# Performance work log

Hardware: AMD Instinct MI355X
Metric: run time of the kernel (lower is better)

## Reference

```python
import jax, jax.numpy as jnp
import numpy as np

N_EMBED = 192
N_HEAD = 6
HEAD_DIM = N_EMBED // N_HEAD  # 32


def setup_inputs() -> dict:
    key = jax.random.key(0)
    k1, k2, k3, k4, k5 = jax.random.split(key, 5)
    B, T = 2048, 128
    scale_qkv = 1.0 / np.sqrt(N_EMBED)
    return {
        "x": jax.random.normal(k1, (B, T, N_EMBED), dtype=jnp.float32),
        "w_qkv": jax.random.normal(k2, (N_EMBED, 3 * N_EMBED), dtype=jnp.float32) * scale_qkv,
        "b_qkv": jax.random.normal(k3, (3 * N_EMBED,), dtype=jnp.float32) * 0.01,
        "w_proj": jax.random.normal(k4, (N_EMBED, N_EMBED), dtype=jnp.float32) * scale_qkv,
        "b_proj": jax.random.normal(k5, (N_EMBED,), dtype=jnp.float32) * 0.01,
    }


def reference(x, w_qkv, b_qkv, w_proj, b_proj):
    B, T, C = x.shape
    qkv = x @ w_qkv + b_qkv                       # [B, T, 3C]
    q, k, v = jnp.split(qkv, 3, axis=-1)
    # [B, H, T, D]
    def heads(t):
        return t.reshape(B, T, N_HEAD, HEAD_DIM).transpose(0, 2, 1, 3)
    q, k, v = heads(q), heads(k), heads(v)
    att = jnp.einsum("bhtd,bhsd->bhts", q, k) / np.sqrt(HEAD_DIM).astype(x.dtype)
    causal = jnp.tril(jnp.ones((T, T), dtype=bool))
    att = jnp.where(causal, att, jnp.finfo(att.dtype).min)
    att = jax.nn.softmax(att, axis=-1)
    # dropout is identity in eval mode
    y = jnp.einsum("bhts,bhsd->bhtd", att, v)      # [B, H, T, D]
    y = y.transpose(0, 2, 1, 3).reshape(B, T, C)
    return y @ w_proj + b_proj
```

## Files before the change

kernel.cpp:

```cpp
#include <hip/hip_runtime.h>
#include <hip/hip_bf16.h>

#define T_  128
#define C_  192
#define H_  6
#define C3_ 576
#define SLAB_ELEMS (96 * 192)
#define SLAB_BYTES (SLAB_ELEMS * 2)

typedef __bf16 bf16x8 __attribute__((ext_vector_type(8)));
typedef __bf16 bf16x4 __attribute__((ext_vector_type(4)));
typedef float  f32x4  __attribute__((ext_vector_type(4)));
typedef unsigned short u16;

__global__ void prep_weights(const float* __restrict__ w_qkv,
                             const float* __restrict__ w_proj,
                             u16* __restrict__ wt)
{
    int idx = blockIdx.x * 256 + threadIdx.x;
    if (idx >= 8 * SLAB_ELEMS) return;
    int slab = idx / SLAB_ELEMS;
    int rem  = idx % SLAB_ELEMS;
    int nl   = rem / 192;
    int kkp  = rem % 192;
    int d    = kkp ^ ((nl & 7) << 3);
    int kt   = d >> 5;
    int e    = d & 31;
    int g    = e >> 3;
    int r    = e & 7;
    int hi   = r >> 2;
    int i    = r & 3;
    int k    = kt * 32 + hi * 16 + g * 4 + i;
    float v;
    if (slab < 6) {
        int sec = nl >> 5;
        int col = sec * C_ + slab * 32 + (nl & 31);
        v = w_qkv[(size_t)k * C3_ + col];
    } else {
        int col = (slab - 6) * 96 + nl;
        v = w_proj[(size_t)k * C_ + col];
    }
    __bf16 bv = (__bf16)v;
    wt[idx] = *reinterpret_cast<u16*>(&bv);
}

__device__ __forceinline__ bf16x8 ld_frag(const __bf16* p) {
    union { bf16x8 v; struct { bf16x4 lo, hi; } s; } u;
    u.s.lo = *reinterpret_cast<const bf16x4*>(p);
    u.s.hi = *reinterpret_cast<const bf16x4*>(p + 16);
    return u.v;
}

__device__ __forceinline__ bf16x8 ld_w(const __bf16* wl, int nl, int kt, int g) {
    return *reinterpret_cast<const bf16x8*>(
        &wl[nl * 192 + (((kt << 5) + (g << 3)) ^ ((nl & 7) << 3))]);
}

__device__ __forceinline__ void stage_slab(const u16* __restrict__ src, u16* dst,
                                           int wid, int lane) {
    #pragma unroll
    for (int p = 0; p < 4; ++p) {
        int off = p * 4096 + wid * 512;
        __builtin_amdgcn_global_load_lds(
            (const __attribute__((address_space(1))) void*)(src + off + lane * 8),
            (__attribute__((address_space(3))) void*)(dst + off), 16, 0, 0);
    }
    if (wid < 4) {
        int off = 16384 + wid * 512;
        __builtin_amdgcn_global_load_lds(
            (const __attribute__((address_space(1))) void*)(src + off + lane * 8),
            (__attribute__((address_space(3))) void*)(dst + off), 16, 0, 0);
    }
}

__global__ __launch_bounds__(512, 4) void attn_fused(
    const float* __restrict__ x,
    const u16*   __restrict__ wt,
    const float* __restrict__ b_qkv,
    const float* __restrict__ b_proj,
    float* __restrict__ y)
{
    __shared__ __align__(16) u16   w_lds[SLAB_ELEMS];
    __shared__ __align__(16) __bf16 k_s[128][40];
    __shared__ __align__(16) __bf16 vt_s[32][136];

    const __bf16* wl = reinterpret_cast<const __bf16*>(w_lds);

    const int b    = blockIdx.x;
    const int tid  = threadIdx.x;
    const int wid  = tid >> 6;
    const int lane = tid & 63;
    const int li   = lane & 15;
    const int g    = lane >> 4;
    const int trow = 16 * wid;
    const int tq   = trow + li;

    const float scale = 0.17677669529663687f;

    stage_slab(wt, w_lds, wid, lane);

    bf16x8 xf[6];
    {
        const float* xr = x + ((size_t)b * T_ + tq) * C_;
        #pragma unroll
        for (int kt = 0; kt < 6; ++kt) {
            f32x4 a0 = *reinterpret_cast<const f32x4*>(xr + kt*32 + 4*g);
            f32x4 a1 = *reinterpret_cast<const f32x4*>(xr + kt*32 + 16 + 4*g);
            bf16x8 f;
            f[0] = (__bf16)a0[0]; f[1] = (__bf16)a0[1]; f[2] = (__bf16)a0[2]; f[3] = (__bf16)a0[3];
            f[4] = (__bf16)a1[0]; f[5] = (__bf16)a1[1]; f[6] = (__bf16)a1[2]; f[7] = (__bf16)a1[3];
            xf[kt] = f;
        }
    }

    bf16x8 of[6];

    #pragma unroll
    for (int h = 0; h < H_; ++h) {
        __syncthreads();

        f32x4 qacc0, qacc1;
        #pragma unroll
        for (int nt = 0; nt < 6; ++nt) {
            const int sec = nt >> 1;
            const int nl  = nt * 16 + li;
            f32x4 acc = *reinterpret_cast<const f32x4*>(
                &b_qkv[sec * C_ + h * 32 + (nt & 1) * 16 + 4 * g]);
            #pragma unroll
            for (int kt = 0; kt < 6; ++kt)
                acc = __builtin_amdgcn_mfma_f32_16x16x32_bf16(ld_w(wl, nl, kt, g),
                                                              xf[kt], acc, 0, 0, 0);
            if (nt == 0)      qacc0 = acc;
            else if (nt == 1) qacc1 = acc;
            else if (nt < 4) {
                bf16x4 pk;
                pk[0]=(__bf16)acc[0]; pk[1]=(__bf16)acc[1]; pk[2]=(__bf16)acc[2]; pk[3]=(__bf16)acc[3];
                *reinterpret_cast<bf16x4*>(&k_s[tq][(nt & 1)*16 + 4*g]) = pk;
            } else {
                #pragma unroll
                for (int r = 0; r < 4; ++r)
                    vt_s[(nt & 1)*16 + 4*g + r][tq] = (__bf16)acc[r];
            }
        }
        bf16x8 qf;
        #pragma unroll
        for (int j = 0; j < 4; ++j) {
            qf[j]     = (__bf16)qacc0[j];
            qf[4 + j] = (__bf16)qacc1[j];
        }
        __syncthreads();

        stage_slab(wt + (h + 1) * SLAB_ELEMS, w_lds, wid, lane);

        float l = 0.f;
        f32x4 o0 = {0.f,0.f,0.f,0.f}, o1 = {0.f,0.f,0.f,0.f};
        #pragma unroll
        for (int hh = 0; hh < 2; ++hh) {
            if (hh == 1 && wid < 4) break;
            f32x4 sacc[4];
            #pragma unroll
            for (int j = 0; j < 4; ++j) {
                bf16x8 kf = ld_frag(&k_s[(hh*4 + j)*16 + li][4*g]);
                f32x4 z = {0.f, 0.f, 0.f, 0.f};
                sacc[j] = __builtin_amdgcn_mfma_f32_16x16x32_bf16(kf, qf, z, 0, 0, 0);
            }
            #pragma unroll
            for (int j = 0; j < 4; ++j) {
                #pragma unroll
                for (int r = 0; r < 4; ++r) {
                    const int key = (hh*4 + j)*16 + 4*g + r;
                    float p = (key <= tq) ? __expf(sacc[j][r] * scale) : 0.f;
                    sacc[j][r] = p;
                    l += p;
                }
            }
            #pragma unroll
            for (int kp = 0; kp < 2; ++kp) {
                bf16x8 pf;
                #pragma unroll
                for (int j2 = 0; j2 < 4; ++j2) {
                    pf[j2]     = (__bf16)sacc[2*kp][j2];
                    pf[4 + j2] = (__bf16)sacc[2*kp + 1][j2];
                }
                bf16x8 vf0 = ld_frag(&vt_s[li     ][(hh*2 + kp)*32 + 4*g]);
                bf16x8 vf1 = ld_frag(&vt_s[16 + li][(hh*2 + kp)*32 + 4*g]);
                o0 = __builtin_amdgcn_mfma_f32_16x16x32_bf16(vf0, pf, o0, 0, 0, 0);
                o1 = __builtin_amdgcn_mfma_f32_16x16x32_bf16(vf1, pf, o1, 0, 0, 0);
            }
        }
        l += __shfl_xor(l, 16);
        l += __shfl_xor(l, 32);
        const float rl = 1.f / l;
        #pragma unroll
        for (int j = 0; j < 4; ++j) {
            of[h][j]     = (__bf16)(o0[j] * rl);
            of[h][4 + j] = (__bf16)(o1[j] * rl);
        }
    }

    float* yr = y + (size_t)b * T_ * C_;
    #pragma unroll
    for (int chunk = 0; chunk < 2; ++chunk) {
        __syncthreads();
        #pragma unroll
        for (int nt = 0; nt < 6; ++nt) {
            const int nl = nt * 16 + li;
            f32x4 acc = *reinterpret_cast<const f32x4*>(
                &b_proj[chunk * 96 + nt*16 + 4*g]);
            #pragma unroll
            for (int kt = 0; kt < 6; ++kt)
                acc = __builtin_amdgcn_mfma_f32_16x16x32_bf16(ld_w(wl, nl, kt, g),
                                                              of[kt], acc, 0, 0, 0);
            *reinterpret_cast<f32x4*>(&yr[(size_t)tq * C_ + chunk*96 + nt*16 + 4*g]) = acc;
        }
        if (chunk == 0) {
            __syncthreads();
            stage_slab(wt + 7 * SLAB_ELEMS, w_lds, wid, lane);
        }
    }
}

extern "C" void kernel_launch(void* const* d_in, const int* in_sizes, int n_in,
                              void* d_out, int out_size, void* d_ws, size_t ws_size,
                              hipStream_t stream) {
    const float* x      = (const float*)d_in[0];
    const float* w_qkv  = (const float*)d_in[1];
    const float* b_qkv  = (const float*)d_in[2];
    const float* w_proj = (const float*)d_in[3];
    const float* b_proj = (const float*)d_in[4];
    float* yv = (float*)d_out;
    u16*   wt = (u16*)d_ws;
    const int B = in_sizes[0] / (T_ * C_);

    prep_weights<<<(8 * SLAB_ELEMS + 255) / 256, 256, 0, stream>>>(w_qkv, w_proj, wt);
    attn_fused<<<B, 512, 0, stream>>>(x, wt, b_qkv, b_proj, yv);
}
```

Measured before the change: 181.3 us.

## Skip fully-masked key tiles per wave and fold softmax scale into Q with exp2

The attention loop now works on 16-key tiles in pairs and stops at the wave's diagonal tile, so it no longer computes QK^T, exp and PV for keys that are fully masked. The causal mask is applied only on the diagonal tile. The softmax scale times log2(e) is folded into Q before the bf16 conversion, and the exp uses the raw v_exp_f32 instruction. Two independent output accumulators are used to split the MFMA dependency chains. Rounding Q after scaling slightly changes numerics, and the wave-dependent trip count makes waves within a block less balanced.

Result: slower. 219.9 us (+21.3%).

```diff
diff --git a/kernel.cpp b/kernel.cpp
--- a/kernel.cpp
+++ b/kernel.cpp
@@ -56,6 +56,12 @@
         &wl[nl * 192 + (((kt << 5) + (g << 3)) ^ ((nl & 7) << 3))]);
 }
 
+__device__ __forceinline__ float fexp2(float x) {
+    float r;
+    asm("v_exp_f32 %0, %1" : "=v"(r) : "v"(x));
+    return r;
+}
+
 __device__ __forceinline__ void stage_slab(const u16* __restrict__ src, u16* dst,
                                            int wid, int lane) {
     #pragma unroll
@@ -95,7 +101,7 @@
     const int trow = 16 * wid;
     const int tq   = trow + li;
 
-    const float scale = 0.17677669529663687f;
+    const float scale2 = 0.25503482459546f;
 
     stage_slab(wt, w_lds, wid, lane);
 
@@ -145,47 +151,54 @@
         bf16x8 qf;
         #pragma unroll
         for (int j = 0; j < 4; ++j) {
-            qf[j]     = (__bf16)qacc0[j];
-            qf[4 + j] = (__bf16)qacc1[j];
+            qf[j]     = (__bf16)(qacc0[j] * scale2);
+            qf[4 + j] = (__bf16)(qacc1[j] * scale2);
         }
         __syncthreads();
 
         stage_slab(wt + (h + 1) * SLAB_ELEMS, w_lds, wid, lane);
 
         float l = 0.f;
-        f32x4 o0 = {0.f,0.f,0.f,0.f}, o1 = {0.f,0.f,0.f,0.f};
-        #pragma unroll
-        for (int hh = 0; hh < 2; ++hh) {
-            if (hh == 1 && wid < 4) break;
-            f32x4 sacc[4];
+        f32x4 oa0 = {0.f,0.f,0.f,0.f}, oa1 = {0.f,0.f,0.f,0.f};
+        f32x4 ob0 = {0.f,0.f,0.f,0.f}, ob1 = {0.f,0.f,0.f,0.f};
+        #pragma unroll
+        for (int jp = 0; jp < 4; ++jp) {
+            const int ta = 2*jp, tb = 2*jp + 1;
+            if (ta > wid) break;
+            const bool hasb = (tb <= wid);
+            f32x4 z = {0.f, 0.f, 0.f, 0.f};
+            bf16x8 kfa = ld_frag(&k_s[ta*16 + li][4*g]);
+            f32x4 sa = __builtin_amdgcn_mfma_f32_16x16x32_bf16(kfa, qf, z, 0, 0, 0);
+            f32x4 sb;
+            if (hasb) {
+                bf16x8 kfb = ld_frag(&k_s[tb*16 + li][4*g]);
+                sb = __builtin_amdgcn_mfma_f32_16x16x32_bf16(kfb, qf, z, 0, 0, 0);
+            }
+            bf16x8 pf;
             #pragma unroll
-            for (int j = 0; j < 4; ++j) {
-                bf16x8 kf = ld_frag(&k_s[(hh*4 + j)*16 + li][4*g]);
-                f32x4 z = {0.f, 0.f, 0.f, 0.f};
-                sacc[j] = __builtin_amdgcn_mfma_f32_16x16x32_bf16(kf, qf, z, 0, 0, 0);
-            }
-            #pragma unroll
-            for (int j = 0; j < 4; ++j) {
-                #pragma unroll
-                for (int r = 0; r < 4; ++r) {
-                    const int key = (hh*4 + j)*16 + 4*g + r;
-                    float p = (key <= tq) ? __expf(sacc[j][r] * scale) : 0.f;
-                    sacc[j][r] = p;
-                    l += p;
+            for (int r = 0; r < 4; ++r) {
+                float pa = fexp2(sa[r]);
+                if (ta == wid)
+                    pa = (ta*16 + 4*g + r <= tq) ? pa : 0.f;
+                l += pa;
+                pf[r] = (__bf16)pa;
+                float pb = 0.f;
+                if (hasb) {
+                    pb = fexp2(sb[r]);
+                    if (tb == wid)
+                        pb = (tb*16 + 4*g + r <= tq) ? pb : 0.f;
+                    l += pb;
                 }
-            }
-            #pragma unroll
-            for (int kp = 0; kp < 2; ++kp) {
-                bf16x8 pf;
-                #pragma unroll
-                for (int j2 = 0; j2 < 4; ++j2) {
-                    pf[j2]     = (__bf16)sacc[2*kp][j2];
-                    pf[4 + j2] = (__bf16)sacc[2*kp + 1][j2];
-                }
-                bf16x8 vf0 = ld_frag(&vt_s[li     ][(hh*2 + kp)*32 + 4*g]);
-                bf16x8 vf1 = ld_frag(&vt_s[16 + li][(hh*2 + kp)*32 + 4*g]);
-                o0 = __builtin_amdgcn_mfma_f32_16x16x32_bf16(vf0, pf, o0, 0, 0, 0);
-                o1 = __builtin_amdgcn_mfma_f32_16x16x32_bf16(vf1, pf, o1, 0, 0, 0);
+                pf[4 + r] = (__bf16)pb;
+            }
+            bf16x8 vf0 = ld_frag(&vt_s[li     ][jp*32 + 4*g]);
+            bf16x8 vf1 = ld_frag(&vt_s[16 + li][jp*32 + 4*g]);
+            if (jp & 1) {
+                ob0 = __builtin_amdgcn_mfma_f32_16x16x32_bf16(vf0, pf, ob0, 0, 0, 0);
+                ob1 = __builtin_amdgcn_mfma_f32_16x16x32_bf16(vf1, pf, ob1, 0, 0, 0);
+            } else {
+                oa0 = __builtin_amdgcn_mfma_f32_16x16x32_bf16(vf0, pf, oa0, 0, 0, 0);
+                oa1 = __builtin_amdgcn_mfma_f32_16x16x32_bf16(vf1, pf, oa1, 0, 0, 0);
             }
         }
         l += __shfl_xor(l, 16);
@@ -193,8 +206,8 @@
         const float rl = 1.f / l;
         #pragma unroll
         for (int j = 0; j < 4; ++j) {
-            of[h][j]     = (__bf16)(o0[j] * rl);
-            of[h][4 + j] = (__bf16)(o1[j] * rl);
+            of[h][j]     = (__bf16)((oa0[j] + ob0[j]) * rl);
+            of[h][4 + j] = (__bf16)((oa1[j] + ob1[j]) * rl);
         }
     }
 
```

## Give each wave two query row tiles and skip fully masked causal tiles

Applied to the files above, without the earlier changes.

Drops the block size from 512 to 256 threads so each wave handles 32 rows (two 16-row M tiles). Every weight fragment read from LDS now feeds two MFMAs, which halves LDS weight traffic per output. Score and PV tiles that lie entirely above the causal diagonal are skipped, and the softmax scale is folded into Q before the QK product. The trade-off is roughly twice the registers per thread, which may cut occupancy, and fewer waves to hide latency within each block.

Measured after the change: 186.4 us. 2.8% more time.

```diff
diff --git a/kernel.cpp b/kernel.cpp
--- a/kernel.cpp
+++ b/kernel.cpp
@@ -59,21 +59,15 @@
 __device__ __forceinline__ void stage_slab(const u16* __restrict__ src, u16* dst,
                                            int wid, int lane) {
     #pragma unroll
-    for (int p = 0; p < 4; ++p) {
-        int off = p * 4096 + wid * 512;
+    for (int p = 0; p < 9; ++p) {
+        int off = p * 2048 + wid * 512;
         __builtin_amdgcn_global_load_lds(
             (const __attribute__((address_space(1))) void*)(src + off + lane * 8),
             (__attribute__((address_space(3))) void*)(dst + off), 16, 0, 0);
     }
-    if (wid < 4) {
-        int off = 16384 + wid * 512;
-        __builtin_amdgcn_global_load_lds(
-            (const __attribute__((address_space(1))) void*)(src + off + lane * 8),
-            (__attribute__((address_space(3))) void*)(dst + off), 16, 0, 0);
-    }
-}
-
-__global__ __launch_bounds__(512, 4) void attn_fused(
+}
+
+__global__ __launch_bounds__(256, 2) void attn_fused(
     const float* __restrict__ x,
     const u16*   __restrict__ wt,
     const float* __restrict__ b_qkv,
@@ -92,16 +86,15 @@
     const int lane = tid & 63;
     const int li   = lane & 15;
     const int g    = lane >> 4;
-    const int trow = 16 * wid;
-    const int tq   = trow + li;
 
     const float scale = 0.17677669529663687f;
 
     stage_slab(wt, w_lds, wid, lane);
 
-    bf16x8 xf[6];
-    {
-        const float* xr = x + ((size_t)b * T_ + tq) * C_;
+    bf16x8 xf[2][6];
+    #pragma unroll
+    for (int m = 0; m < 2; ++m) {
+        const float* xr = x + ((size_t)b * T_ + 32*wid + 16*m + li) * C_;
         #pragma unroll
         for (int kt = 0; kt < 6; ++kt) {
             f32x4 a0 = *reinterpret_cast<const f32x4*>(xr + kt*32 + 4*g);
@@ -109,92 +102,138 @@
             bf16x8 f;
             f[0] = (__bf16)a0[0]; f[1] = (__bf16)a0[1]; f[2] = (__bf16)a0[2]; f[3] = (__bf16)a0[3];
             f[4] = (__bf16)a1[0]; f[5] = (__bf16)a1[1]; f[6] = (__bf16)a1[2]; f[7] = (__bf16)a1[3];
-            xf[kt] = f;
-        }
-    }
-
-    bf16x8 of[6];
+            xf[m][kt] = f;
+        }
+    }
+
+    bf16x8 of[2][6];
 
     #pragma unroll
     for (int h = 0; h < H_; ++h) {
         __syncthreads();
 
-        f32x4 qacc0, qacc1;
+        f32x4 qacc[2][2];
         #pragma unroll
         for (int nt = 0; nt < 6; ++nt) {
             const int sec = nt >> 1;
             const int nl  = nt * 16 + li;
-            f32x4 acc = *reinterpret_cast<const f32x4*>(
+            f32x4 bias = *reinterpret_cast<const f32x4*>(
                 &b_qkv[sec * C_ + h * 32 + (nt & 1) * 16 + 4 * g]);
-            #pragma unroll
-            for (int kt = 0; kt < 6; ++kt)
-                acc = __builtin_amdgcn_mfma_f32_16x16x32_bf16(ld_w(wl, nl, kt, g),
-                                                              xf[kt], acc, 0, 0, 0);
-            if (nt == 0)      qacc0 = acc;
-            else if (nt == 1) qacc1 = acc;
-            else if (nt < 4) {
-                bf16x4 pk;
-                pk[0]=(__bf16)acc[0]; pk[1]=(__bf16)acc[1]; pk[2]=(__bf16)acc[2]; pk[3]=(__bf16)acc[3];
-                *reinterpret_cast<bf16x4*>(&k_s[tq][(nt & 1)*16 + 4*g]) = pk;
+            f32x4 acc0 = bias, acc1 = bias;
+            #pragma unroll
+            for (int kt = 0; kt < 6; ++kt) {
+                bf16x8 wf = ld_w(wl, nl, kt, g);
+                acc0 = __builtin_amdgcn_mfma_f32_16x16x32_bf16(wf, xf[0][kt], acc0, 0, 0, 0);
+                acc1 = __builtin_amdgcn_mfma_f32_16x16x32_bf16(wf, xf[1][kt], acc1, 0, 0, 0);
+            }
+            if (nt < 2) {
+                qacc[0][nt] = acc0;
+                qacc[1][nt] = acc1;
+            } else if (nt < 4) {
+                bf16x4 pk0, pk1;
+                #pragma unroll
+                for (int j = 0; j < 4; ++j) { pk0[j]=(__bf16)acc0[j]; pk1[j]=(__bf16)acc1[j]; }
+                *reinterpret_cast<bf16x4*>(&k_s[32*wid      + li][(nt & 1)*16 + 4*g]) = pk0;
+                *reinterpret_cast<bf16x4*>(&k_s[32*wid + 16 + li][(nt & 1)*16 + 4*g]) = pk1;
             } else {
                 #pragma unroll
-                for (int r = 0; r < 4; ++r)
-                    vt_s[(nt & 1)*16 + 4*g + r][tq] = (__bf16)acc[r];
-            }
-        }
-        bf16x8 qf;
-        #pragma unroll
-        for (int j = 0; j < 4; ++j) {
-            qf[j]     = (__bf16)qacc0[j];
-            qf[4 + j] = (__bf16)qacc1[j];
-        }
+                for (int r = 0; r < 4; ++r) {
+                    vt_s[(nt & 1)*16 + 4*g + r][32*wid      + li] = (__bf16)acc0[r];
+                    vt_s[(nt & 1)*16 + 4*g + r][32*wid + 16 + li] = (__bf16)acc1[r];
+                }
+            }
+        }
+        bf16x8 qf[2];
+        #pragma unroll
+        for (int m = 0; m < 2; ++m)
+            #pragma unroll
+            for (int j = 0; j < 4; ++j) {
+                qf[m][j]     = (__bf16)(qacc[m][0][j] * scale);
+                qf[m][4 + j] = (__bf16)(qacc[m][1][j] * scale);
+            }
         __syncthreads();
 
         stage_slab(wt + (h + 1) * SLAB_ELEMS, w_lds, wid, lane);
 
-        float l = 0.f;
-        f32x4 o0 = {0.f,0.f,0.f,0.f}, o1 = {0.f,0.f,0.f,0.f};
+        f32x4 lv[2];
+        f32x4 oacc[2][2];
+        #pragma unroll
+        for (int m = 0; m < 2; ++m) {
+            lv[m] = f32x4{0.f, 0.f, 0.f, 0.f};
+            oacc[m][0] = f32x4{0.f, 0.f, 0.f, 0.f};
+            oacc[m][1] = f32x4{0.f, 0.f, 0.f, 0.f};
+        }
         #pragma unroll
         for (int hh = 0; hh < 2; ++hh) {
-            if (hh == 1 && wid < 4) break;
-            f32x4 sacc[4];
+            if (hh == 1 && wid < 2) break;
+            f32x4 sacc[2][4];
             #pragma unroll
             for (int j = 0; j < 4; ++j) {
-                bf16x8 kf = ld_frag(&k_s[(hh*4 + j)*16 + li][4*g]);
+                const int tile = hh*4 + j;
+                if (tile > 2*wid + 1) {
+                    sacc[0][j] = f32x4{0.f,0.f,0.f,0.f};
+                    sacc[1][j] = f32x4{0.f,0.f,0.f,0.f};
+                    continue;
+                }
+                bf16x8 kf = ld_frag(&k_s[tile*16 + li][4*g]);
                 f32x4 z = {0.f, 0.f, 0.f, 0.f};
-                sacc[j] = __builtin_amdgcn_mfma_f32_16x16x32_bf16(kf, qf, z, 0, 0, 0);
-            }
-            #pragma unroll
-            for (int j = 0; j < 4; ++j) {
-                #pragma unroll
-                for (int r = 0; r < 4; ++r) {
-                    const int key = (hh*4 + j)*16 + 4*g + r;
-                    float p = (key <= tq) ? __expf(sacc[j][r] * scale) : 0.f;
-                    sacc[j][r] = p;
-                    l += p;
+                sacc[0][j] = __builtin_amdgcn_mfma_f32_16x16x32_bf16(kf, qf[0], z, 0, 0, 0);
+                sacc[1][j] = __builtin_amdgcn_mfma_f32_16x16x32_bf16(kf, qf[1], z, 0, 0, 0);
+            }
+            #pragma unroll
+            for (int m = 0; m < 2; ++m) {
+                const int rt = 2*wid + m;
+                #pragma unroll
+                for (int j = 0; j < 4; ++j) {
+                    const int tile = hh*4 + j;
+                    if (tile > rt) {
+                        sacc[m][j] = f32x4{0.f,0.f,0.f,0.f};
+                    } else if (tile == rt) {
+                        #pragma unroll
+                        for (int r = 0; r < 4; ++r) {
+                            float p = (4*g + r <= li) ? __expf(sacc[m][j][r]) : 0.f;
+                            sacc[m][j][r] = p;
+                            lv[m][r] += p;
+                        }
+                    } else {
+                        #pragma unroll
+                        for (int r = 0; r < 4; ++r) {
+                            float p = __expf(sacc[m][j][r]);
+                            sacc[m][j][r] = p;
+                            lv[m][r] += p;
+                        }
+                    }
                 }
             }
             #pragma unroll
             for (int kp = 0; kp < 2; ++kp) {
-                bf16x8 pf;
-                #pragma unroll
-                for (int j2 = 0; j2 < 4; ++j2) {
-                    pf[j2]     = (__bf16)sacc[2*kp][j2];
-                    pf[4 + j2] = (__bf16)sacc[2*kp + 1][j2];
-                }
+                if (hh*4 + 2*kp > 2*wid + 1) break;
                 bf16x8 vf0 = ld_frag(&vt_s[li     ][(hh*2 + kp)*32 + 4*g]);
                 bf16x8 vf1 = ld_frag(&vt_s[16 + li][(hh*2 + kp)*32 + 4*g]);
-                o0 = __builtin_amdgcn_mfma_f32_16x16x32_bf16(vf0, pf, o0, 0, 0, 0);
-                o1 = __builtin_amdgcn_mfma_f32_16x16x32_bf16(vf1, pf, o1, 0, 0, 0);
-            }
-        }
-        l += __shfl_xor(l, 16);
-        l += __shfl_xor(l, 32);
-        const float rl = 1.f / l;
-        #pragma unroll
-        for (int j = 0; j < 4; ++j) {
-            of[h][j]     = (__bf16)(o0[j] * rl);
-            of[h][4 + j] = (__bf16)(o1[j] * rl);
+                #pragma unroll
+                for (int m = 0; m < 2; ++m) {
+                    bf16x8 pf;
+                    #pragma unroll
+                    for (int j2 = 0; j2 < 4; ++j2) {
+                        pf[j2]     = (__bf16)sacc[m][2*kp][j2];
+                        pf[4 + j2] = (__bf16)sacc[m][2*kp + 1][j2];
+                    }
+                    oacc[m][0] = __builtin_amdgcn_mfma_f32_16x16x32_bf16(vf0, pf, oacc[m][0], 0, 0, 0);
+                    oacc[m][1] = __builtin_amdgcn_mfma_f32_16x16x32_bf16(vf1, pf, oacc[m][1], 0, 0, 0);
+                }
+            }
+        }
+        #pragma unroll
+        for (int m = 0; m < 2; ++m) {
+            float l = (lv[m][0] + lv[m][1]) + (lv[m][2] + lv[m][3]);
+            l += __shfl_xor(l, 16);
+            l += __shfl_xor(l, 32);
+            const float rl = 1.f / l;
+            #pragma unroll
+            for (int j = 0; j < 4; ++j) {
+                of[m][h][j]     = (__bf16)(oacc[m][0][j] * rl);
+                of[m][h][4 + j] = (__bf16)(oacc[m][1][j] * rl);
+            }
         }
     }
 
@@ -205,13 +244,17 @@
         #pragma unroll
         for (int nt = 0; nt < 6; ++nt) {
             const int nl = nt * 16 + li;
-            f32x4 acc = *reinterpret_cast<const f32x4*>(
+            f32x4 bias = *reinterpret_cast<const f32x4*>(
                 &b_proj[chunk * 96 + nt*16 + 4*g]);
-            #pragma unroll
-            for (int kt = 0; kt < 6; ++kt)
-                acc = __builtin_amdgcn_mfma_f32_16x16x32_bf16(ld_w(wl, nl, kt, g),
-                                                              of[kt], acc, 0, 0, 0);
-            *reinterpret_cast<f32x4*>(&yr[(size_t)tq * C_ + chunk*96 + nt*16 + 4*g]) = acc;
+            f32x4 acc0 = bias, acc1 = bias;
+            #pragma unroll
+            for (int kt = 0; kt < 6; ++kt) {
+                bf16x8 wf = ld_w(wl, nl, kt, g);
+                acc0 = __builtin_amdgcn_mfma_f32_16x16x32_bf16(wf, of[0][kt], acc0, 0, 0, 0);
+                acc1 = __builtin_amdgcn_mfma_f32_16x16x32_bf16(wf, of[1][kt], acc1, 0, 0, 0);
+            }
+            *reinterpret_cast<f32x4*>(&yr[(size_t)(32*wid      + li) * C_ + chunk*96 + nt*16 + 4*g]) = acc0;
+            *reinterpret_cast<f32x4*>(&yr[(size_t)(32*wid + 16 + li) * C_ + chunk*96 + nt*16 + 4*g]) = acc1;
         }
         if (chunk == 0) {
             __syncthreads();
@@ -233,5 +276,5 @@
     const int B = in_sizes[0] / (T_ * C_);
 
     prep_weights<<<(8 * SLAB_ELEMS + 255) / 256, 256, 0, stream>>>(w_qkv, w_proj, wt);
-    attn_fused<<<B, 512, 0, stream>>>(x, wt, b_qkv, b_proj, yv);
-}
+    attn_fused<<<B, 256, 0, stream>>>(x, wt, b_qkv, b_proj, yv);
+}
```

## Read weights directly from global in fragment order, double-buffer K/V, skip masked PV

Applied to the files above, without the earlier changes.

Weights are pre-permuted so each MFMA fragment is a contiguous 16-byte per-lane global load, which removes LDS staging of weight slabs and the barriers tied to it. K and V^T shared buffers are double-buffered by head parity, so one barrier per head suffices. PV MFMAs for fully masked key blocks are skipped. The trade is higher global/L2 traffic for weights on every block in exchange for fewer barriers and lower LDS use, which may raise occupancy.

Result: slower. 296.1 us (+63.3%).

```diff
diff --git a/kernel.cpp b/kernel.cpp
--- a/kernel.cpp
+++ b/kernel.cpp
@@ -5,8 +5,7 @@
 #define C_  192
 #define H_  6
 #define C3_ 576
-#define SLAB_ELEMS (96 * 192)
-#define SLAB_BYTES (SLAB_ELEMS * 2)
+#define SLAB_ELEMS (6 * 6 * 64 * 8)
 
 typedef __bf16 bf16x8 __attribute__((ext_vector_type(8)));
 typedef __bf16 bf16x4 __attribute__((ext_vector_type(4)));
@@ -21,16 +20,15 @@
     if (idx >= 8 * SLAB_ELEMS) return;
     int slab = idx / SLAB_ELEMS;
     int rem  = idx % SLAB_ELEMS;
-    int nl   = rem / 192;
-    int kkp  = rem % 192;
-    int d    = kkp ^ ((nl & 7) << 3);
-    int kt   = d >> 5;
-    int e    = d & 31;
-    int g    = e >> 3;
-    int r    = e & 7;
-    int hi   = r >> 2;
-    int i    = r & 3;
-    int k    = kt * 32 + hi * 16 + g * 4 + i;
+    int j    = rem & 7;
+    int lane = (rem >> 3) & 63;
+    int grp  = rem >> 9;
+    int kt   = grp / 6;
+    int nt   = grp % 6;
+    int li   = lane & 15;
+    int g    = lane >> 4;
+    int nl   = nt * 16 + li;
+    int k    = kt * 32 + (j >> 2) * 16 + g * 4 + (j & 3);
     float v;
     if (slab < 6) {
         int sec = nl >> 5;
@@ -51,26 +49,9 @@
     return u.v;
 }
 
-__device__ __forceinline__ bf16x8 ld_w(const __bf16* wl, int nl, int kt, int g) {
-    return *reinterpret_cast<const bf16x8*>(
-        &wl[nl * 192 + (((kt << 5) + (g << 3)) ^ ((nl & 7) << 3))]);
-}
-
-__device__ __forceinline__ void stage_slab(const u16* __restrict__ src, u16* dst,
-                                           int wid, int lane) {
-    #pragma unroll
-    for (int p = 0; p < 4; ++p) {
-        int off = p * 4096 + wid * 512;
-        __builtin_amdgcn_global_load_lds(
-            (const __attribute__((address_space(1))) void*)(src + off + lane * 8),
-            (__attribute__((address_space(3))) void*)(dst + off), 16, 0, 0);
-    }
-    if (wid < 4) {
-        int off = 16384 + wid * 512;
-        __builtin_amdgcn_global_load_lds(
-            (const __attribute__((address_space(1))) void*)(src + off + lane * 8),
-            (__attribute__((address_space(3))) void*)(dst + off), 16, 0, 0);
-    }
+__device__ __forceinline__ bf16x8 ld_w(const u16* __restrict__ ws,
+                                       int kt, int nt, int lane) {
+    return *reinterpret_cast<const bf16x8*>(ws + ((kt * 6 + nt) << 9) + lane * 8);
 }
 
 __global__ __launch_bounds__(512, 4) void attn_fused(
@@ -80,11 +61,8 @@
     const float* __restrict__ b_proj,
     float* __restrict__ y)
 {
-    __shared__ __align__(16) u16   w_lds[SLAB_ELEMS];
-    __shared__ __align__(16) __bf16 k_s[128][40];
-    __shared__ __align__(16) __bf16 vt_s[32][136];
-
-    const __bf16* wl = reinterpret_cast<const __bf16*>(w_lds);
+    __shared__ __align__(16) __bf16 k_s[2][128][40];
+    __shared__ __align__(16) __bf16 vt_s[2][32][136];
 
     const int b    = blockIdx.x;
     const int tid  = threadIdx.x;
@@ -97,8 +75,6 @@
 
     const float scale = 0.17677669529663687f;
 
-    stage_slab(wt, w_lds, wid, lane);
-
     bf16x8 xf[6];
     {
         const float* xr = x + ((size_t)b * T_ + tq) * C_;
@@ -117,29 +93,29 @@
 
     #pragma unroll
     for (int h = 0; h < H_; ++h) {
-        __syncthreads();
+        const u16* ws = wt + h * SLAB_ELEMS;
+        const int  buf = h & 1;
 
         f32x4 qacc0, qacc1;
         #pragma unroll
         for (int nt = 0; nt < 6; ++nt) {
             const int sec = nt >> 1;
-            const int nl  = nt * 16 + li;
             f32x4 acc = *reinterpret_cast<const f32x4*>(
                 &b_qkv[sec * C_ + h * 32 + (nt & 1) * 16 + 4 * g]);
             #pragma unroll
             for (int kt = 0; kt < 6; ++kt)
-                acc = __builtin_amdgcn_mfma_f32_16x16x32_bf16(ld_w(wl, nl, kt, g),
+                acc = __builtin_amdgcn_mfma_f32_16x16x32_bf16(ld_w(ws, kt, nt, lane),
                                                               xf[kt], acc, 0, 0, 0);
             if (nt == 0)      qacc0 = acc;
             else if (nt == 1) qacc1 = acc;
             else if (nt < 4) {
                 bf16x4 pk;
                 pk[0]=(__bf16)acc[0]; pk[1]=(__bf16)acc[1]; pk[2]=(__bf16)acc[2]; pk[3]=(__bf16)acc[3];
-                *reinterpret_cast<bf16x4*>(&k_s[tq][(nt & 1)*16 + 4*g]) = pk;
+                *reinterpret_cast<bf16x4*>(&k_s[buf][tq][(nt & 1)*16 + 4*g]) = pk;
             } else {
                 #pragma unroll
                 for (int r = 0; r < 4; ++r)
-                    vt_s[(nt & 1)*16 + 4*g + r][tq] = (__bf16)acc[r];
+                    vt_s[buf][(nt & 1)*16 + 4*g + r][tq] = (__bf16)acc[r];
             }
         }
         bf16x8 qf;
@@ -150,8 +126,6 @@
         }
         __syncthreads();
 
-        stage_slab(wt + (h + 1) * SLAB_ELEMS, w_lds, wid, lane);
-
         float l = 0.f;
         f32x4 o0 = {0.f,0.f,0.f,0.f}, o1 = {0.f,0.f,0.f,0.f};
         #pragma unroll
@@ -160,7 +134,7 @@
             f32x4 sacc[4];
             #pragma unroll
             for (int j = 0; j < 4; ++j) {
-                bf16x8 kf = ld_frag(&k_s[(hh*4 + j)*16 + li][4*g]);
+                bf16x8 kf = ld_frag(&k_s[buf][(hh*4 + j)*16 + li][4*g]);
                 f32x4 z = {0.f, 0.f, 0.f, 0.f};
                 sacc[j] = __builtin_amdgcn_mfma_f32_16x16x32_bf16(kf, qf, z, 0, 0, 0);
             }
@@ -176,14 +150,15 @@
             }
             #pragma unroll
             for (int kp = 0; kp < 2; ++kp) {
+                if (hh*4 + 2*kp > wid) break;
                 bf16x8 pf;
                 #pragma unroll
                 for (int j2 = 0; j2 < 4; ++j2) {
                     pf[j2]     = (__bf16)sacc[2*kp][j2];
                     pf[4 + j2] = (__bf16)sacc[2*kp + 1][j2];
                 }
-                bf16x8 vf0 = ld_frag(&vt_s[li     ][(hh*2 + kp)*32 + 4*g]);
-                bf16x8 vf1 = ld_frag(&vt_s[16 + li][(hh*2 + kp)*32 + 4*g]);
+                bf16x8 vf0 = ld_frag(&vt_s[buf][li     ][(hh*2 + kp)*32 + 4*g]);
+                bf16x8 vf1 = ld_frag(&vt_s[buf][16 + li][(hh*2 + kp)*32 + 4*g]);
                 o0 = __builtin_amdgcn_mfma_f32_16x16x32_bf16(vf0, pf, o0, 0, 0, 0);
                 o1 = __builtin_amdgcn_mfma_f32_16x16x32_bf16(vf1, pf, o1, 0, 0, 0);
             }
@@ -201,21 +176,16 @@
     float* yr = y + (size_t)b * T_ * C_;
     #pragma unroll
     for (int chunk = 0; chunk < 2; ++chunk) {
-        __syncthreads();
+        const u16* ws = wt + (6 + chunk) * SLAB_ELEMS;
         #pragma unroll
         for (int nt = 0; nt < 6; ++nt) {
-            const int nl = nt * 16 + li;
             f32x4 acc = *reinterpret_cast<const f32x4*>(
                 &b_proj[chunk * 96 + nt*16 + 4*g]);
             #pragma unroll
             for (int kt = 0; kt < 6; ++kt)
-                acc = __builtin_amdgcn_mfma_f32_16x16x32_bf16(ld_w(wl, nl, kt, g),
+                acc = __builtin_amdgcn_mfma_f32_16x16x32_bf16(ld_w(ws, kt, nt, lane),
                                                               of[kt], acc, 0, 0, 0);
             *reinterpret_cast<f32x4*>(&yr[(size_t)tq * C_ + chunk*96 + nt*16 + 4*g]) = acc;
-        }
-        if (chunk == 0) {
-            __syncthreads();
-            stage_slab(wt + 7 * SLAB_ELEMS, w_lds, wid, lane);
         }
     }
 }
```
